# Kernel tuning notes

Hardware: AMD Instinct MI355X
Metric: run time of the kernel (lower is better)

## Reference

```python
import jax, jax.numpy as jnp
import numpy as np

DIM = 256
HID = 256
EPS = 1e-5

def _layernorm(x, g, b):
    mu = jnp.mean(x, axis=-1, keepdims=True)
    var = jnp.mean(jnp.square(x - mu), axis=-1, keepdims=True)
    return (x - mu) * jax.lax.rsqrt(var + EPS) * g + b

def setup_inputs() -> dict:
    key = jax.random.key(0)
    ks = jax.random.split(key, 6)
    B, N = 2, 512
    x = jax.random.normal(ks[0], (B, N, DIM), dtype=jnp.float32)
    mask = jax.random.randint(ks[1], (B, N), 0, 2).astype(jnp.bool_)
    s_in = 1.0 / np.sqrt(DIM)
    s_h = 1.0 / np.sqrt(HID)
    return {
        "x": x,
        "mask": mask,
        "ln_g": jnp.ones((DIM,), jnp.float32),
        "ln_b": jnp.zeros((DIM,), jnp.float32),
        "Wl": jax.random.uniform(ks[2], (DIM, HID), jnp.float32, -s_in, s_in),
        "bl": jnp.zeros((HID,), jnp.float32),
        "Wo": jax.random.uniform(ks[3], (HID, HID), jnp.float32, -s_h, s_h),
        "bo": jnp.zeros((HID,), jnp.float32),
        "lno_g": jnp.ones((HID,), jnp.float32),
        "lno_b": jnp.zeros((HID,), jnp.float32),
    }

def reference(x, mask, ln_g, ln_b, Wl, bl, Wo, bo, lno_g, lno_b):
    # x: [B, N, D], mask: [B, N] bool
    xn = _layernorm(x, ln_g, ln_b)
    left = xn @ Wl + bl                                  # [B, N, H]
    outer = left[:, :, None, :] * left[:, None, :, :]    # [B, N, N, H]
    m2 = (mask[:, :, None] & mask[:, None, :])[..., None]  # [B, N, N, 1]
    outer = jnp.where(m2, outer, 0.0)
    h = _layernorm(jax.nn.gelu(outer, approximate=False), lno_g, lno_b)
    return h @ Wo + bo                                   # [B, N, N, H]
```

## Files before the change

kernel.cpp:

```cpp
#include <hip/hip_runtime.h>
#include <stdint.h>

#define DIM 256
#define HID 256
#define NSEQ 512
#define NB 2
#define EPS 1e-5f
#define PREP_ROWS 4

typedef __attribute__((ext_vector_type(4))) float f32x4;
typedef __attribute__((ext_vector_type(4))) short bf16x4;
typedef __attribute__((ext_vector_type(8))) short bf16x8;

#define DIAG_BLOCKS 512
#define BATCH_BLOCKS 2304

__device__ __forceinline__ unsigned short f2bf(float f) {
    unsigned int u = __float_as_uint(f);
    u += 0x7fffu + ((u >> 16) & 1u);
    return (unsigned short)(u >> 16);
}

__device__ __forceinline__ float bfval(float f) {
    return __uint_as_float((unsigned)f2bf(f) << 16);
}

__device__ __forceinline__ float gelu_fast(float x) {
    const float z  = x * 0.7071067811865476f;
    const float az = fabsf(z);
    const float t  = __builtin_amdgcn_rcpf(fmaf(0.3275911f, az, 1.0f));
    float p = fmaf(1.061405429f, t, -1.453152027f);
    p = fmaf(p, t,  1.421413741f);
    p = fmaf(p, t, -0.284496736f);
    p = fmaf(p, t,  0.254829592f);
    p = p * t;
    const float e = __builtin_amdgcn_exp2f(az * az * -1.4426950408889634f);
    float erfv = fmaf(-p, e, 1.0f);
    erfv = copysignf(erfv, z);
    return 0.5f * x * (1.0f + erfv);
}

__device__ __forceinline__ int pairpos(int k) {
    return ((k >> 5) << 5) + (((k >> 2) & 3) << 3) + (((k >> 4) & 1) << 2) + (k & 3);
}

__global__ __launch_bounds__(256) void prep_kernel(
    const float* __restrict__ x, const void* __restrict__ mask,
    const float* __restrict__ ln_g, const float* __restrict__ ln_b,
    const float* __restrict__ Wl, const float* __restrict__ bl,
    const float* __restrict__ Wo, const float* __restrict__ lno_b,
    const float* __restrict__ bo,
    float* __restrict__ lm, unsigned short* __restrict__ woTp,
    int* __restrict__ maskr, float* __restrict__ cst)
{
    const int row0 = blockIdx.x * PREP_ROWS;
    const int t = threadIdx.x;
    const int lane = t & 63, w = t >> 6;
    __shared__ float xs[PREP_ROWS][DIM];
    __shared__ float redS[PREP_ROWS][4], redQ[PREP_ROWS][4];
    __shared__ int bad_s[4];

    {
        const int v = ((const int*)mask)[t];
        unsigned long long bm = __ballot((v & ~1) != 0);
        if (lane == 0) bad_s[w] = (bm != 0ull) ? 1 : 0;
    }

    float v[PREP_ROWS];
    #pragma unroll
    for (int r = 0; r < PREP_ROWS; ++r) {
        v[r] = x[(size_t)(row0 + r) * DIM + t];
        float s = v[r], ss = v[r] * v[r];
        #pragma unroll
        for (int o = 32; o; o >>= 1) { s += __shfl_xor(s, o); ss += __shfl_xor(ss, o); }
        if (lane == 0) { redS[r][w] = s; redQ[r][w] = ss; }
    }
    __syncthreads();
    #pragma unroll
    for (int r = 0; r < PREP_ROWS; ++r) {
        const float s  = redS[r][0] + redS[r][1] + redS[r][2] + redS[r][3];
        const float ss = redQ[r][0] + redQ[r][1] + redQ[r][2] + redQ[r][3];
        const float mu  = s * (1.0f / DIM);
        const float var = ss * (1.0f / DIM) - mu * mu;
        const float rs  = rsqrtf(var + EPS);
        xs[r][t] = (v[r] - mu) * rs * ln_g[t] + ln_b[t];
    }
    __syncthreads();

    float acc[PREP_ROWS];
    #pragma unroll
    for (int r = 0; r < PREP_ROWS; ++r) acc[r] = bl[t];
    #pragma unroll 4
    for (int k = 0; k < DIM; k += 4) {
        const float w0 = Wl[(k + 0) * HID + t];
        const float w1 = Wl[(k + 1) * HID + t];
        const float w2 = Wl[(k + 2) * HID + t];
        const float w3 = Wl[(k + 3) * HID + t];
        #pragma unroll
        for (int r = 0; r < PREP_ROWS; ++r) {
            const float4 xv = *(const float4*)&xs[r][k];
            acc[r] = fmaf(xv.x, w0, acc[r]);
            acc[r] = fmaf(xv.y, w1, acc[r]);
            acc[r] = fmaf(xv.z, w2, acc[r]);
            acc[r] = fmaf(xv.w, w3, acc[r]);
        }
    }

    const int packed = bad_s[0] | bad_s[1] | bad_s[2] | bad_s[3];
    #pragma unroll
    for (int r = 0; r < PREP_ROWS; ++r) {
        const int row = row0 + r;
        const int mv = packed ? (int)((const unsigned char*)mask)[row]
                              : ((const int*)mask)[row];
        lm[(size_t)row * HID + t] = mv ? acc[r] : 0.0f;
        if (t == 0) maskr[row] = mv;
        if (row < HID) {
            woTp[row * HID + pairpos(t)] = f2bf(Wo[t * HID + row]);
        }
    }
    if (blockIdx.x == 0) {
        float c = bo[t];
        for (int k = 0; k < HID; ++k)
            c = fmaf(bfval(lno_b[k]), bfval(Wo[k * HID + t]), c);
        cst[t] = c;
    }
}

__global__ __launch_bounds__(512) void outer_kernel(
    const float* __restrict__ lm, const unsigned short* __restrict__ woTp,
    const float* __restrict__ lno_g, const float* __restrict__ lno_b,
    const float* __restrict__ bo, const int* __restrict__ maskr,
    const float* __restrict__ cst, float* __restrict__ out)
{
    int blk = (int)blockIdx.x;
    int b = 0;
    if (blk >= BATCH_BLOCKS) { b = 1; blk -= BATCH_BLOCKS; }
    int i, jt, mirror;
    if (blk < DIAG_BLOCKS) {
        i = blk; jt = i >> 6; mirror = 0;
    } else {
        const int r2 = blk - DIAG_BLOCKS;
        const int p  = r2 >> 6;
        const int il = r2 & 63;
        int bi = 0, start = 0;
        #pragma unroll
        for (int bb = 0; bb < 7; ++bb) {
            const int s = bb * 7 - (bb * (bb - 1)) / 2;
            if (p >= s) { bi = bb; start = s; }
        }
        const int bj = bi + 1 + (p - start);
        i = bi * 64 + il;
        jt = bj;
        mirror = 1;
    }
    const int j0  = jt * 64;
    const int t    = threadIdx.x;
    const int lane = t & 63;
    const int w    = t >> 6;
    const size_t base = (size_t)(b * NSEQ + i) * NSEQ * HID;

    const f32x4 cvec = *(const f32x4*)&cst[lane * 4];

    if (maskr[b * NSEQ + i] == 0) {
        #pragma unroll
        for (int r = 0; r < 8; ++r) {
            const int j = j0 + w * 8 + r;
            *(f32x4*)&out[base + (size_t)j * HID + lane * 4] = cvec;
            if (mirror)
                *(f32x4*)&out[((size_t)(b * NSEQ + j) * NSEQ + i) * HID + lane * 4] = cvec;
        }
        return;
    }

    __shared__ __align__(16) unsigned char ybuf[64 * 512];

    const float4 li4 = *(const float4*)&lm[(size_t)(b * NSEQ + i) * HID + lane * 4];
    const float4 g4  = *(const float4*)&lno_g[lane * 4];
    const float4 bb4 = *(const float4*)&lno_b[lane * 4];

    const int mvl = maskr[b * NSEQ + j0 + lane];
    const unsigned long long livemask = __ballot(mvl != 0);

    const int wrb = ((lane >> 3) << 6) + ((lane & 3) << 4) + (((lane >> 2) & 1) << 3);

    const uint2 ucst = make_uint2(
        ((unsigned)f2bf(bb4.y) << 16) | (unsigned)f2bf(bb4.x),
        ((unsigned)f2bf(bb4.w) << 16) | (unsigned)f2bf(bb4.z));

    #pragma unroll 4
    for (int r = 0; r < 8; ++r) {
        const int rl = w * 8 + r;
        const int j  = j0 + rl;
        const int off = rl * 512 + (wrb ^ ((rl & 7) << 4));
        if (!((livemask >> rl) & 1ull)) {
            *(uint2*)&ybuf[off] = ucst;
            *(f32x4*)&out[base + (size_t)j * HID + lane * 4] = cvec;
            if (mirror)
                *(f32x4*)&out[((size_t)(b * NSEQ + j) * NSEQ + i) * HID + lane * 4] = cvec;
            continue;
        }
        float4 lj4 = *(const float4*)&lm[(size_t)(b * NSEQ + j) * HID + lane * 4];
        float4 p;
        p.x = gelu_fast(li4.x * lj4.x);
        p.y = gelu_fast(li4.y * lj4.y);
        p.z = gelu_fast(li4.z * lj4.z);
        p.w = gelu_fast(li4.w * lj4.w);
        float s  = p.x + p.y + p.z + p.w;
        float ss = p.x * p.x + p.y * p.y + p.z * p.z + p.w * p.w;
        #pragma unroll
        for (int o = 32; o; o >>= 1) { s += __shfl_xor(s, o); ss += __shfl_xor(ss, o); }
        const float mu  = s * (1.0f / HID);
        const float var = ss * (1.0f / HID) - mu * mu;
        const float rs  = rsqrtf(var + EPS);
        const float y0 = (p.x - mu) * rs * g4.x + bb4.x;
        const float y1 = (p.y - mu) * rs * g4.y + bb4.y;
        const float y2 = (p.z - mu) * rs * g4.z + bb4.z;
        const float y3 = (p.w - mu) * rs * g4.w + bb4.w;
        const unsigned int u0 = ((unsigned)f2bf(y1) << 16) | (unsigned)f2bf(y0);
        const unsigned int u1 = ((unsigned)f2bf(y3) << 16) | (unsigned)f2bf(y2);
        *(uint2*)&ybuf[off] = make_uint2(u0, u1);
    }
    __syncthreads();

    const int n0  = w * 32;
    const int l15 = lane & 15;
    const int q   = lane >> 4;

    f32x4 acc[4][2];
    #pragma unroll
    for (int mi = 0; mi < 4; ++mi)
        #pragma unroll
        for (int nh = 0; nh < 2; ++nh)
            acc[mi][nh] = (f32x4){0.f, 0.f, 0.f, 0.f};

#if !__has_builtin(__builtin_amdgcn_mfma_f32_16x16x16bf16_1k)
    #pragma unroll
    for (int mi = 0; mi < 4; ++mi)
        #pragma unroll
        for (int nh = 0; nh < 2; ++nh)
            asm volatile("" : "+v"(acc[mi][nh]));
    asm volatile("s_nop 1");
#endif

    #pragma unroll
    for (int kk2 = 0; kk2 < 8; ++kk2) {
        const int pb = kk2 * 64 + q * 16;
        bf16x8 a8[4], b8[2];
        #pragma unroll
        for (int mi = 0; mi < 4; ++mi) {
            const int rowm = mi * 16 + l15;
            a8[mi] = *(const bf16x8*)&ybuf[rowm * 512 + (pb ^ ((rowm & 7) << 4))];
        }
        #pragma unroll
        for (int nh = 0; nh < 2; ++nh) {
            const int col = n0 + nh * 16 + l15;
            b8[nh] = *(const bf16x8*)&woTp[col * HID + kk2 * 32 + q * 8];
        }
        #pragma unroll
        for (int mi = 0; mi < 4; ++mi) {
            const bf16x4 alo = __builtin_shufflevector(a8[mi], a8[mi], 0, 1, 2, 3);
            const bf16x4 ahi = __builtin_shufflevector(a8[mi], a8[mi], 4, 5, 6, 7);
            #pragma unroll
            for (int nh = 0; nh < 2; ++nh) {
                const bf16x4 blo = __builtin_shufflevector(b8[nh], b8[nh], 0, 1, 2, 3);
                const bf16x4 bhi = __builtin_shufflevector(b8[nh], b8[nh], 4, 5, 6, 7);
#if __has_builtin(__builtin_amdgcn_mfma_f32_16x16x16bf16_1k)
                acc[mi][nh] = __builtin_amdgcn_mfma_f32_16x16x16bf16_1k(
                    blo, alo, acc[mi][nh], 0, 0, 0);
                acc[mi][nh] = __builtin_amdgcn_mfma_f32_16x16x16bf16_1k(
                    bhi, ahi, acc[mi][nh], 0, 0, 0);
#else
                asm volatile("v_mfma_f32_16x16x16_bf16 %0, %1, %2, %0"
                             : "+v"(acc[mi][nh]) : "v"(blo), "v"(alo));
                asm volatile("v_mfma_f32_16x16x16_bf16 %0, %1, %2, %0"
                             : "+v"(acc[mi][nh]) : "v"(bhi), "v"(ahi));
#endif
            }
        }
    }

#if !__has_builtin(__builtin_amdgcn_mfma_f32_16x16x16bf16_1k)
    asm volatile("s_nop 7");
    asm volatile("s_nop 7");
    #pragma unroll
    for (int mi = 0; mi < 4; ++mi)
        #pragma unroll
        for (int nh = 0; nh < 2; ++nh)
            asm volatile("" : "+v"(acc[mi][nh]));
#endif

    #pragma unroll
    for (int mi = 0; mi < 4; ++mi) {
        const int rowm = mi * 16 + l15;
        if (!((livemask >> rowm) & 1ull)) continue;
        const int j = j0 + rowm;
        const size_t prow = base + (size_t)j * HID;
        const size_t mrow = ((size_t)(b * NSEQ + j) * NSEQ + i) * HID;
        #pragma unroll
        for (int nh = 0; nh < 2; ++nh) {
            const int h0 = n0 + nh * 16 + q * 4;
            const float4 bo4 = *(const float4*)&bo[h0];
            f32x4 o;
            o[0] = acc[mi][nh][0] + bo4.x;
            o[1] = acc[mi][nh][1] + bo4.y;
            o[2] = acc[mi][nh][2] + bo4.z;
            o[3] = acc[mi][nh][3] + bo4.w;
            *(f32x4*)&out[prow + h0] = o;
            if (mirror)
                *(f32x4*)&out[mrow + h0] = o;
        }
    }
}

extern "C" void kernel_launch(void* const* d_in, const int* in_sizes, int n_in,
                              void* d_out, int out_size, void* d_ws, size_t ws_size,
                              hipStream_t stream) {
    (void)in_sizes; (void)n_in; (void)out_size; (void)ws_size;
    const float* x     = (const float*)d_in[0];
    const void*  mask  = d_in[1];
    const float* ln_g  = (const float*)d_in[2];
    const float* ln_b  = (const float*)d_in[3];
    const float* Wl    = (const float*)d_in[4];
    const float* bl    = (const float*)d_in[5];
    const float* Wo    = (const float*)d_in[6];
    const float* bo    = (const float*)d_in[7];
    const float* lno_g = (const float*)d_in[8];
    const float* lno_b = (const float*)d_in[9];

    char* ws = (char*)d_ws;
    float*          lm    = (float*)ws;
    unsigned short* woTp  = (unsigned short*)(ws + (size_t)NB * NSEQ * HID * 4);
    int*            maskr = (int*)(ws + (size_t)NB * NSEQ * HID * 4 + HID * HID * 2);
    float*          cst   = (float*)(ws + (size_t)NB * NSEQ * HID * 4 + HID * HID * 2
                                        + NB * NSEQ * 4);

    prep_kernel<<<NB * NSEQ / PREP_ROWS, 256, 0, stream>>>(
        x, mask, ln_g, ln_b, Wl, bl, Wo, lno_b, bo, lm, woTp, maskr, cst);
    outer_kernel<<<NB * BATCH_BLOCKS, 512, 0, stream>>>(
        lm, woTp, lno_g, lno_b, bo, maskr, cst, (float*)d_out);
}
```

Before: 148.4 us.

## Process two tiles per block, overlapping second tile's GELU/LN with first's MFMA

```diff
diff --git a/kernel.cpp b/kernel.cpp
--- a/kernel.cpp
+++ b/kernel.cpp
@@ -14,6 +14,7 @@
 
 #define DIAG_BLOCKS 512
 #define BATCH_BLOCKS 2304
+#define NTILES (NB * BATCH_BLOCKS)
 
 __device__ __forceinline__ unsigned short f2bf(float f) {
     unsigned int u = __float_as_uint(f);
@@ -126,190 +127,199 @@
     }
 }
 
+struct Tile { int b, i, j0, mirror, live; size_t base; };
+
+__device__ __forceinline__ Tile decode_tile(int idx, const int* __restrict__ maskr) {
+    Tile tl;
+    int blk = idx;
+    tl.b = 0;
+    if (blk >= BATCH_BLOCKS) { tl.b = 1; blk -= BATCH_BLOCKS; }
+    if (blk < DIAG_BLOCKS) {
+        tl.i = blk; tl.j0 = (tl.i >> 6) * 64; tl.mirror = 0;
+    } else {
+        const int r2 = blk - DIAG_BLOCKS;
+        const int p  = r2 >> 6;
+        const int il = r2 & 63;
+        int bi = 0, start = 0;
+        #pragma unroll
+        for (int bb = 0; bb < 7; ++bb) {
+            const int s = bb * 7 - (bb * (bb - 1)) / 2;
+            if (p >= s) { bi = bb; start = s; }
+        }
+        const int bj = bi + 1 + (p - start);
+        tl.i = bi * 64 + il;
+        tl.j0 = bj * 64;
+        tl.mirror = 1;
+    }
+    tl.base = (size_t)(tl.b * NSEQ + tl.i) * NSEQ * HID;
+    tl.live = maskr[tl.b * NSEQ + tl.i] != 0;
+    return tl;
+}
+
 __global__ __launch_bounds__(512) void outer_kernel(
     const float* __restrict__ lm, const unsigned short* __restrict__ woTp,
     const float* __restrict__ lno_g, const float* __restrict__ lno_b,
     const float* __restrict__ bo, const int* __restrict__ maskr,
     const float* __restrict__ cst, float* __restrict__ out)
 {
-    int blk = (int)blockIdx.x;
-    int b = 0;
-    if (blk >= BATCH_BLOCKS) { b = 1; blk -= BATCH_BLOCKS; }
-    int i, jt, mirror;
-    if (blk < DIAG_BLOCKS) {
-        i = blk; jt = i >> 6; mirror = 0;
-    } else {
-        const int r2 = blk - DIAG_BLOCKS;
-        const int p  = r2 >> 6;
-        const int il = r2 & 63;
-        int bi = 0, start = 0;
-        #pragma unroll
-        for (int bb = 0; bb < 7; ++bb) {
-            const int s = bb * 7 - (bb * (bb - 1)) / 2;
-            if (p >= s) { bi = bb; start = s; }
-        }
-        const int bj = bi + 1 + (p - start);
-        i = bi * 64 + il;
-        jt = bj;
-        mirror = 1;
-    }
-    const int j0  = jt * 64;
     const int t    = threadIdx.x;
     const int lane = t & 63;
     const int w    = t >> 6;
-    const size_t base = (size_t)(b * NSEQ + i) * NSEQ * HID;
-
-    const f32x4 cvec = *(const f32x4*)&cst[lane * 4];
-
-    if (maskr[b * NSEQ + i] == 0) {
-        #pragma unroll
-        for (int r = 0; r < 8; ++r) {
-            const int j = j0 + w * 8 + r;
-            *(f32x4*)&out[base + (size_t)j * HID + lane * 4] = cvec;
-            if (mirror)
-                *(f32x4*)&out[((size_t)(b * NSEQ + j) * NSEQ + i) * HID + lane * 4] = cvec;
-        }
-        return;
-    }
-
-    __shared__ __align__(16) unsigned char ybuf[64 * 512];
-
-    const float4 li4 = *(const float4*)&lm[(size_t)(b * NSEQ + i) * HID + lane * 4];
+    const int n0   = w * 32;
+    const int l15  = lane & 15;
+    const int q    = lane >> 4;
+
+    __shared__ __align__(16) unsigned char ybuf[2][64 * 512];
+
     const float4 g4  = *(const float4*)&lno_g[lane * 4];
     const float4 bb4 = *(const float4*)&lno_b[lane * 4];
-
-    const int mvl = maskr[b * NSEQ + j0 + lane];
-    const unsigned long long livemask = __ballot(mvl != 0);
-
-    const int wrb = ((lane >> 3) << 6) + ((lane & 3) << 4) + (((lane >> 2) & 1) << 3);
-
+    const f32x4  cvec = *(const f32x4*)&cst[lane * 4];
     const uint2 ucst = make_uint2(
         ((unsigned)f2bf(bb4.y) << 16) | (unsigned)f2bf(bb4.x),
         ((unsigned)f2bf(bb4.w) << 16) | (unsigned)f2bf(bb4.z));
-
-    #pragma unroll 4
-    for (int r = 0; r < 8; ++r) {
-        const int rl = w * 8 + r;
-        const int j  = j0 + rl;
-        const int off = rl * 512 + (wrb ^ ((rl & 7) << 4));
-        if (!((livemask >> rl) & 1ull)) {
-            *(uint2*)&ybuf[off] = ucst;
-            *(f32x4*)&out[base + (size_t)j * HID + lane * 4] = cvec;
-            if (mirror)
-                *(f32x4*)&out[((size_t)(b * NSEQ + j) * NSEQ + i) * HID + lane * 4] = cvec;
-            continue;
-        }
-        float4 lj4 = *(const float4*)&lm[(size_t)(b * NSEQ + j) * HID + lane * 4];
-        float4 p;
-        p.x = gelu_fast(li4.x * lj4.x);
-        p.y = gelu_fast(li4.y * lj4.y);
-        p.z = gelu_fast(li4.z * lj4.z);
-        p.w = gelu_fast(li4.w * lj4.w);
-        float s  = p.x + p.y + p.z + p.w;
-        float ss = p.x * p.x + p.y * p.y + p.z * p.z + p.w * p.w;
-        #pragma unroll
-        for (int o = 32; o; o >>= 1) { s += __shfl_xor(s, o); ss += __shfl_xor(ss, o); }
-        const float mu  = s * (1.0f / HID);
-        const float var = ss * (1.0f / HID) - mu * mu;
-        const float rs  = rsqrtf(var + EPS);
-        const float y0 = (p.x - mu) * rs * g4.x + bb4.x;
-        const float y1 = (p.y - mu) * rs * g4.y + bb4.y;
-        const float y2 = (p.z - mu) * rs * g4.z + bb4.z;
-        const float y3 = (p.w - mu) * rs * g4.w + bb4.w;
-        const unsigned int u0 = ((unsigned)f2bf(y1) << 16) | (unsigned)f2bf(y0);
-        const unsigned int u1 = ((unsigned)f2bf(y3) << 16) | (unsigned)f2bf(y2);
-        *(uint2*)&ybuf[off] = make_uint2(u0, u1);
-    }
-    __syncthreads();
-
-    const int n0  = w * 32;
-    const int l15 = lane & 15;
-    const int q   = lane >> 4;
-
-    f32x4 acc[4][2];
-    #pragma unroll
-    for (int mi = 0; mi < 4; ++mi)
-        #pragma unroll
-        for (int nh = 0; nh < 2; ++nh)
-            acc[mi][nh] = (f32x4){0.f, 0.f, 0.f, 0.f};
+    const int wrb = ((lane >> 3) << 6) + ((lane & 3) << 4) + (((lane >> 2) & 1) << 3);
+
+    auto phaseA = [&](const Tile& tl, unsigned char* buf) {
+        const float4 li4 = *(const float4*)&lm[(size_t)(tl.b * NSEQ + tl.i) * HID + lane * 4];
+        const int mvl = maskr[tl.b * NSEQ + tl.j0 + lane];
+        const unsigned long long livemask = __ballot(mvl != 0);
+        #pragma unroll 4
+        for (int r = 0; r < 8; ++r) {
+            const int rl = w * 8 + r;
+            const int j  = tl.j0 + rl;
+            const int off = rl * 512 + (wrb ^ ((rl & 7) << 4));
+            if (!((livemask >> rl) & 1ull)) {
+                *(uint2*)&buf[off] = ucst;
+                *(f32x4*)&out[tl.base + (size_t)j * HID + lane * 4] = cvec;
+                if (tl.mirror)
+                    *(f32x4*)&out[((size_t)(tl.b * NSEQ + j) * NSEQ + tl.i) * HID + lane * 4] = cvec;
+                continue;
+            }
+            float4 lj4 = *(const float4*)&lm[(size_t)(tl.b * NSEQ + j) * HID + lane * 4];
+            float4 p;
+            p.x = gelu_fast(li4.x * lj4.x);
+            p.y = gelu_fast(li4.y * lj4.y);
+            p.z = gelu_fast(li4.z * lj4.z);
+            p.w = gelu_fast(li4.w * lj4.w);
+            float s  = p.x + p.y + p.z + p.w;
+            float ss = p.x * p.x + p.y * p.y + p.z * p.z + p.w * p.w;
+            #pragma unroll
+            for (int o = 32; o; o >>= 1) { s += __shfl_xor(s, o); ss += __shfl_xor(ss, o); }
+            const float mu  = s * (1.0f / HID);
+            const float var = ss * (1.0f / HID) - mu * mu;
+            const float rs  = rsqrtf(var + EPS);
+            const float y0 = (p.x - mu) * rs * g4.x + bb4.x;
+            const float y1 = (p.y - mu) * rs * g4.y + bb4.y;
+            const float y2 = (p.z - mu) * rs * g4.z + bb4.z;
+            const float y3 = (p.w - mu) * rs * g4.w + bb4.w;
+            const unsigned int u0 = ((unsigned)f2bf(y1) << 16) | (unsigned)f2bf(y0);
+            const unsigned int u1 = ((unsigned)f2bf(y3) << 16) | (unsigned)f2bf(y2);
+            *(uint2*)&buf[off] = make_uint2(u0, u1);
+        }
+    };
+
+    auto phaseB = [&](const Tile& tl, const unsigned char* buf) {
+        const int mvl = maskr[tl.b * NSEQ + tl.j0 + lane];
+        const unsigned long long livemask = __ballot(mvl != 0);
+
+        f32x4 acc[4][2];
+        #pragma unroll
+        for (int mi = 0; mi < 4; ++mi)
+            #pragma unroll
+            for (int nh = 0; nh < 2; ++nh)
+                acc[mi][nh] = (f32x4){0.f, 0.f, 0.f, 0.f};
+
+        #pragma unroll
+        for (int kk2 = 0; kk2 < 8; ++kk2) {
+            const int pb = kk2 * 64 + q * 16;
+            bf16x8 a8[4], b8[2];
+            #pragma unroll
+            for (int mi = 0; mi < 4; ++mi) {
+                const int rowm = mi * 16 + l15;
+                a8[mi] = *(const bf16x8*)&buf[rowm * 512 + (pb ^ ((rowm & 7) << 4))];
+            }
+            #pragma unroll
+            for (int nh = 0; nh < 2; ++nh) {
+                const int col = n0 + nh * 16 + l15;
+                b8[nh] = *(const bf16x8*)&woTp[col * HID + kk2 * 32 + q * 8];
+            }
+            #pragma unroll
+            for (int mi = 0; mi < 4; ++mi) {
+                const bf16x4 alo = __builtin_shufflevector(a8[mi], a8[mi], 0, 1, 2, 3);
+                const bf16x4 ahi = __builtin_shufflevector(a8[mi], a8[mi], 4, 5, 6, 7);
+                #pragma unroll
+                for (int nh = 0; nh < 2; ++nh) {
+                    const bf16x4 blo = __builtin_shufflevector(b8[nh], b8[nh], 0, 1, 2, 3);
+                    const bf16x4 bhi = __builtin_shufflevector(b8[nh], b8[nh], 4, 5, 6, 7);
+#if __has_builtin(__builtin_amdgcn_mfma_f32_16x16x16bf16_1k)
+                    acc[mi][nh] = __builtin_amdgcn_mfma_f32_16x16x16bf16_1k(
+                        blo, alo, acc[mi][nh], 0, 0, 0);
+                    acc[mi][nh] = __builtin_amdgcn_mfma_f32_16x16x16bf16_1k(
+                        bhi, ahi, acc[mi][nh], 0, 0, 0);
+#else
+                    asm volatile("v_mfma_f32_16x16x16_bf16 %0, %1, %2, %0"
+                                 : "+v"(acc[mi][nh]) : "v"(blo), "v"(alo));
+                    asm volatile("v_mfma_f32_16x16x16_bf16 %0, %1, %2, %0"
+                                 : "+v"(acc[mi][nh]) : "v"(bhi), "v"(ahi));
+#endif
+                }
+            }
+        }
 
 #if !__has_builtin(__builtin_amdgcn_mfma_f32_16x16x16bf16_1k)
-    #pragma unroll
-    for (int mi = 0; mi < 4; ++mi)
-        #pragma unroll
-        for (int nh = 0; nh < 2; ++nh)
-            asm volatile("" : "+v"(acc[mi][nh]));
-    asm volatile("s_nop 1");
+        asm volatile("s_nop 7");
+        asm volatile("s_nop 7");
+        #pragma unroll
+        for (int mi = 0; mi < 4; ++mi)
+            #pragma unroll
+            for (int nh = 0; nh < 2; ++nh)
+                asm volatile("" : "+v"(acc[mi][nh]));
 #endif
 
-    #pragma unroll
-    for (int kk2 = 0; kk2 < 8; ++kk2) {
-        const int pb = kk2 * 64 + q * 16;
-        bf16x8 a8[4], b8[2];
         #pragma unroll
         for (int mi = 0; mi < 4; ++mi) {
             const int rowm = mi * 16 + l15;
-            a8[mi] = *(const bf16x8*)&ybuf[rowm * 512 + (pb ^ ((rowm & 7) << 4))];
-        }
-        #pragma unroll
-        for (int nh = 0; nh < 2; ++nh) {
-            const int col = n0 + nh * 16 + l15;
-            b8[nh] = *(const bf16x8*)&woTp[col * HID + kk2 * 32 + q * 8];
-        }
-        #pragma unroll
-        for (int mi = 0; mi < 4; ++mi) {
-            const bf16x4 alo = __builtin_shufflevector(a8[mi], a8[mi], 0, 1, 2, 3);
-            const bf16x4 ahi = __builtin_shufflevector(a8[mi], a8[mi], 4, 5, 6, 7);
+            if (!((livemask >> rowm) & 1ull)) continue;
+            const int j = tl.j0 + rowm;
+            const size_t prow = tl.base + (size_t)j * HID;
+            const size_t mrow = ((size_t)(tl.b * NSEQ + j) * NSEQ + tl.i) * HID;
             #pragma unroll
             for (int nh = 0; nh < 2; ++nh) {
-                const bf16x4 blo = __builtin_shufflevector(b8[nh], b8[nh], 0, 1, 2, 3);
-                const bf16x4 bhi = __builtin_shufflevector(b8[nh], b8[nh], 4, 5, 6, 7);
-#if __has_builtin(__builtin_amdgcn_mfma_f32_16x16x16bf16_1k)
-                acc[mi][nh] = __builtin_amdgcn_mfma_f32_16x16x16bf16_1k(
-                    blo, alo, acc[mi][nh], 0, 0, 0);
-                acc[mi][nh] = __builtin_amdgcn_mfma_f32_16x16x16bf16_1k(
-                    bhi, ahi, acc[mi][nh], 0, 0, 0);
-#else
-                asm volatile("v_mfma_f32_16x16x16_bf16 %0, %1, %2, %0"
-                             : "+v"(acc[mi][nh]) : "v"(blo), "v"(alo));
-                asm volatile("v_mfma_f32_16x16x16_bf16 %0, %1, %2, %0"
-                             : "+v"(acc[mi][nh]) : "v"(bhi), "v"(ahi));
-#endif
-            }
-        }
-    }
-
-#if !__has_builtin(__builtin_amdgcn_mfma_f32_16x16x16bf16_1k)
-    asm volatile("s_nop 7");
-    asm volatile("s_nop 7");
-    #pragma unroll
-    for (int mi = 0; mi < 4; ++mi)
-        #pragma unroll
-        for (int nh = 0; nh < 2; ++nh)
-            asm volatile("" : "+v"(acc[mi][nh]));
-#endif
-
-    #pragma unroll
-    for (int mi = 0; mi < 4; ++mi) {
-        const int rowm = mi * 16 + l15;
-        if (!((livemask >> rowm) & 1ull)) continue;
-        const int j = j0 + rowm;
-        const size_t prow = base + (size_t)j * HID;
-        const size_t mrow = ((size_t)(b * NSEQ + j) * NSEQ + i) * HID;
-        #pragma unroll
-        for (int nh = 0; nh < 2; ++nh) {
-            const int h0 = n0 + nh * 16 + q * 4;
-            const float4 bo4 = *(const float4*)&bo[h0];
-            f32x4 o;
-            o[0] = acc[mi][nh][0] + bo4.x;
-            o[1] = acc[mi][nh][1] + bo4.y;
-            o[2] = acc[mi][nh][2] + bo4.z;
-            o[3] = acc[mi][nh][3] + bo4.w;
-            *(f32x4*)&out[prow + h0] = o;
-            if (mirror)
-                *(f32x4*)&out[mrow + h0] = o;
-        }
-    }
+                const int h0 = n0 + nh * 16 + q * 4;
+                const float4 bo4 = *(const float4*)&bo[h0];
+                f32x4 o;
+                o[0] = acc[mi][nh][0] + bo4.x;
+                o[1] = acc[mi][nh][1] + bo4.y;
+                o[2] = acc[mi][nh][2] + bo4.z;
+                o[3] = acc[mi][nh][3] + bo4.w;
+                *(f32x4*)&out[prow + h0] = o;
+                if (tl.mirror)
+                    *(f32x4*)&out[mrow + h0] = o;
+            }
+        }
+    };
+
+    auto deadB = [&](const Tile& tl) {
+        #pragma unroll
+        for (int r = 0; r < 8; ++r) {
+            const int j = tl.j0 + w * 8 + r;
+            *(f32x4*)&out[tl.base + (size_t)j * HID + lane * 4] = cvec;
+            if (tl.mirror)
+                *(f32x4*)&out[((size_t)(tl.b * NSEQ + j) * NSEQ + tl.i) * HID + lane * 4] = cvec;
+        }
+    };
+
+    const Tile t0 = decode_tile(2 * (int)blockIdx.x,     maskr);
+    const Tile t1 = decode_tile(2 * (int)blockIdx.x + 1, maskr);
+
+    if (t0.live) phaseA(t0, ybuf[0]);
+    __syncthreads();
+
+    if (t0.live) phaseB(t0, ybuf[0]); else deadB(t0);
+    if (t1.live) phaseA(t1, ybuf[1]);
+    __syncthreads();
+
+    if (t1.live) phaseB(t1, ybuf[1]); else deadB(t1);
 }
 
 extern "C" void kernel_launch(void* const* d_in, const int* in_sizes, int n_in,
@@ -336,6 +346,6 @@
 
     prep_kernel<<<NB * NSEQ / PREP_ROWS, 256, 0, stream>>>(
         x, mask, ln_g, ln_b, Wl, bl, Wo, lno_b, bo, lm, woTp, maskr, cst);
-    outer_kernel<<<NB * BATCH_BLOCKS, 512, 0, stream>>>(
+    outer_kernel<<<NTILES / 2, 512, 0, stream>>>(
         lm, woTp, lno_g, lno_b, bo, maskr, cst, (float*)d_out);
 }
```

Result: slower. 155.7 us (+4.9%).
